# Kernel optimization log

Hardware: AMD Instinct MI355X
Metric: run time of the kernel (lower is better)

The kernel has to match this reference:

```python
import jax, jax.numpy as jnp
import numpy as np

K_RATIO = 0.2
EPS = 1e-6


def setup_inputs() -> dict:
    key = jax.random.key(0)
    k1, k2 = jax.random.split(key)
    B, C, D, H, W = 2, 4, 128, 128, 128
    logits = jax.random.normal(k1, (B, C, D, H, W), dtype=jnp.float32)
    labels = jax.random.randint(k2, (B, D, H, W), 0, C)
    # one-hot target along channel axis 1, matching the tensor-path `target` arg
    target = jax.nn.one_hot(labels, C, axis=1, dtype=jnp.float32)
    return {"logits": logits, "target": target}


def reference(logits, target):
    B, C = logits.shape[0], logits.shape[1]

    # ---- Top-K cross entropy (ignore_index=-1 -> all voxels valid) ----
    y = jnp.argmax(target, axis=1)  # [B, D, H, W] int labels
    logp = jax.nn.log_softmax(logits, axis=1)
    # CE per voxel: -logp[b, y, d, h, w]
    ce = -jnp.take_along_axis(logp, y[:, None], axis=1)[:, 0]  # [B, D, H, W]
    ce_flat = ce.reshape(B, -1)  # [B, N]
    N = ce_flat.shape[1]
    k = max(1, int(N * K_RATIO))  # static: all voxels valid, k < N
    topk_vals, _ = jax.lax.top_k(ce_flat, k)  # [B, k]
    topk_loss = jnp.mean(jnp.mean(topk_vals, axis=1))

    # ---- Soft dice (no valid_mask in tensor path) ----
    p = jax.nn.softmax(logits, axis=1)  # [B, C, D, H, W]
    spatial = tuple(range(2, p.ndim))
    num = 2.0 * jnp.sum(p * target, axis=spatial)          # [B, C]
    den = jnp.sum(p + target, axis=spatial) + EPS          # [B, C]
    dice = 1.0 - num / den                                  # [B, C]
    if C > 1:
        dice = dice[:, 1:]  # drop background channel
    dice_loss = jnp.mean(dice)

    return topk_loss + 0.5 * dice_loss
```

## Files before the change

### kernel.cpp

```cpp
#include <hip/hip_runtime.h>
#include <stdint.h>

#define NVOX (1u << 21)
#define NB   2
#define KSEL 419430u
#define TPB  256
#define VPB  2048
#define BPB  ((int)(NVOX / VPB))
#define NBLK (NB * BPB)
#define NCOPY 64
#define NBIN 4096
#define L1SH 19

__device__ __forceinline__ float wred64(float v) {
#pragma unroll
  for (int o = 32; o > 0; o >>= 1) v += __shfl_down(v, o, 64);
  return v;
}

__global__ __launch_bounds__(TPB, 8) void k1_ce_dice_hist(
    const float* __restrict__ logits, const float* __restrict__ target,
    float* __restrict__ ce, uint32_t* __restrict__ hist1,
    float* __restrict__ dice_acc )
{
  __shared__ uint32_t sh[NBIN];
  const int tid = threadIdx.x;
  for (int i = tid; i < NBIN; i += TPB) sh[i] = 0;
  __syncthreads();

  const int blk = blockIdx.x;
  const int b = blk / BPB;
  const size_t v0 = (size_t)(blk % BPB) * VPB;
  const float* lg = logits + (size_t)b * 4 * NVOX + v0;
  const float* tg = target + (size_t)b * 4 * NVOX + v0;
  float* ceb = ce + ((size_t)b << 21) + v0;

  float sp[4] = {0.f,0.f,0.f,0.f}, nm[4] = {0.f,0.f,0.f,0.f}, ct[4] = {0.f,0.f,0.f,0.f};

#pragma unroll 2
  for (int i = tid * 4; i < VPB; i += TPB * 4) {
    float4 L[4], T[4];
#pragma unroll
    for (int c = 0; c < 4; ++c) {
      L[c] = *(const float4*)(lg + (size_t)c * NVOX + i);
      T[c] = *(const float4*)(tg + (size_t)c * NVOX + i);
    }
    float4 CE;
    float* cep = (float*)&CE;
#pragma unroll
    for (int j = 0; j < 4; ++j) {
      float l[4], t[4];
#pragma unroll
      for (int c = 0; c < 4; ++c) {
        l[c] = ((const float*)&L[c])[j];
        t[c] = ((const float*)&T[c])[j];
      }
      float m = fmaxf(fmaxf(l[0], l[1]), fmaxf(l[2], l[3]));
      float e[4]; float s = 0.f;
#pragma unroll
      for (int c = 0; c < 4; ++c) { e[c] = __expf(l[c] - m); s += e[c]; }
      float inv = 1.f / s;
      float lse = __logf(s);
      float ly = l[0]*t[0] + l[1]*t[1] + l[2]*t[2] + l[3]*t[3];
      float cev = (m - ly) + lse;
      cep[j] = cev;
      atomicAdd(&sh[__float_as_uint(cev) >> L1SH], 1u);
#pragma unroll
      for (int c = 0; c < 4; ++c) {
        float p = e[c] * inv;
        sp[c] += p;
        nm[c] += p * t[c];
        ct[c] += t[c];
      }
    }
    *(float4*)(ceb + i) = CE;
  }

#pragma unroll
  for (int c = 0; c < 4; ++c) { sp[c] = wred64(sp[c]); nm[c] = wred64(nm[c]); ct[c] = wred64(ct[c]); }
  if ((tid & 63) == 0) {
    float* dst = dice_acc + ((size_t)(blk & (NCOPY - 1)) * NB + b) * 12;
#pragma unroll
    for (int c = 0; c < 4; ++c) {
      atomicAdd(dst + c,     sp[c]);
      atomicAdd(dst + 4 + c, nm[c]);
      atomicAdd(dst + 8 + c, ct[c]);
    }
  }
  __syncthreads();
  for (int i = tid; i < NBIN; i += TPB) {
    uint32_t cv = sh[i];
    if (cv) atomicAdd(&hist1[b * NBIN + i], cv);
  }
}

__global__ __launch_bounds__(TPB, 8) void k_pass2(
    const float* __restrict__ ce, const uint32_t* __restrict__ b1p,
    uint32_t* __restrict__ hist2, float* __restrict__ sum_above)
{
  __shared__ uint32_t sh[NBIN];
  __shared__ float wsum[TPB / 64];
  const int tid = threadIdx.x;
  for (int i = tid; i < NBIN; i += TPB) sh[i] = 0;
  __syncthreads();

  const int blk = blockIdx.x;
  const int b = blk / BPB;
  const size_t v0 = (size_t)(blk % BPB) * VPB;
  const float* cb = ce + ((size_t)b << 21) + v0;
  const uint32_t b1 = b1p[b];
  float local = 0.f;

#pragma unroll 2
  for (int i = tid * 4; i < VPB; i += TPB * 4) {
    float4 V = *(const float4*)(cb + i);
    const float* vp = (const float*)&V;
#pragma unroll
    for (int j = 0; j < 4; ++j) {
      uint32_t bits = __float_as_uint(vp[j]);
      uint32_t t12 = bits >> L1SH;
      if (t12 > b1) local += vp[j];
      else if (t12 == b1) atomicAdd(&sh[(bits >> 7) & (NBIN - 1)], 1u);
    }
  }

  local = wred64(local);
  if ((tid & 63) == 0) wsum[tid >> 6] = local;
  __syncthreads();
  if (tid == 0) {
    float t = 0.f;
#pragma unroll
    for (int w = 0; w < TPB / 64; ++w) t += wsum[w];
    if (t != 0.f) atomicAdd(&sum_above[b * NCOPY + (blk & (NCOPY - 1))], t);
  }
  for (int i = tid; i < NBIN; i += TPB) {
    uint32_t cv = sh[i];
    if (cv) atomicAdd(&hist2[(size_t)b * NBIN + i], cv);
  }
}

__global__ __launch_bounds__(256) void k_scan1(
    const uint32_t* __restrict__ hist,
    uint32_t* __restrict__ out_b, uint32_t* __restrict__ out_rem)
{
  const int b = blockIdx.x;
  const int tid = threadIdx.x;
  __shared__ uint32_t chunk[256];
  const int per = NBIN >> 8;
  const uint32_t* h = hist + (size_t)b * NBIN;
  uint32_t s = 0;
  for (int j = 0; j < per; ++j) s += h[tid * per + j];
  chunk[tid] = s;
  __syncthreads();
  if (tid == 0) {
    uint32_t k = KSEL, cum = 0;
    int ci = 255;
    for (; ci > 0; --ci) {
      uint32_t c = chunk[ci];
      if (cum + c >= k) break;
      cum += c;
    }
    int bkt = ci * per;
    for (int j = per - 1; j >= 0; --j) {
      uint32_t c = h[ci * per + j];
      if (cum + c >= k) { bkt = ci * per + j; break; }
      cum += c;
    }
    out_b[b] = (uint32_t)bkt;
    out_rem[b] = k - cum;
  }
}

__global__ __launch_bounds__(256) void k_final(
    const uint32_t* __restrict__ hist2, const uint32_t* __restrict__ b1p,
    const uint32_t* __restrict__ rem1, const float* __restrict__ sum_above,
    const float* __restrict__ dice_acc, float* __restrict__ out)
{
  const int tid = threadIdx.x;
  __shared__ uint32_t chunk[256];
  __shared__ uint32_t sbkt, srem;
  __shared__ float wpart[4];
  __shared__ float ts[NB];
  __shared__ float comp[24];
  const int per = NBIN >> 8;

  for (int b = 0; b < NB; ++b) {
    const uint32_t* h = hist2 + (size_t)b * NBIN;
    uint32_t s = 0;
    for (int j = 0; j < per; ++j) s += h[tid * per + j];
    chunk[tid] = s;
    __syncthreads();
    if (tid == 0) {
      uint32_t k = rem1[b], cum = 0;
      int ci = 255;
      for (; ci > 0; --ci) {
        uint32_t c = chunk[ci];
        if (cum + c >= k) break;
        cum += c;
      }
      int bkt = ci * per;
      for (int j = per - 1; j >= 0; --j) {
        uint32_t c = h[ci * per + j];
        if (cum + c >= k) { bkt = ci * per + j; break; }
        cum += c;
      }
      sbkt = (uint32_t)bkt;
      srem = k - cum;
    }
    __syncthreads();
    const uint32_t b1 = b1p[b];
    const int bkt = (int)sbkt;
    float w = 0.f;
    for (int i = tid; i < NBIN; i += 256) {
      if (i > bkt) {
        uint32_t c = h[i];
        if (c) {
          uint32_t bits = (b1 << L1SH) | ((uint32_t)i << 7) | 64u;
          w += (float)c * __uint_as_float(bits);
        }
      }
    }
    w = wred64(w);
    if ((tid & 63) == 0) wpart[tid >> 6] = w;
    __syncthreads();
    if (tid == 0) {
      float sa = 0.f;
      for (int r = 0; r < NCOPY; ++r) sa += sum_above[b * NCOPY + r];
      uint32_t bits = (b1 << L1SH) | ((uint32_t)bkt << 7) | 64u;
      ts[b] = sa + wpart[0] + wpart[1] + wpart[2] + wpart[3]
              + (float)srem * __uint_as_float(bits);
    }
    __syncthreads();
  }

  if (tid < 24) {
    float a = 0.f;
    for (int r = 0; r < NCOPY; ++r) a += dice_acc[(size_t)r * 24 + tid];
    comp[tid] = a;
  }
  __syncthreads();
  if (tid == 0) {
    float dl = 0.f;
#pragma unroll
    for (int b = 0; b < 2; ++b)
#pragma unroll
      for (int c = 1; c < 4; ++c) {
        float sp = comp[b * 12 + c];
        float nm = comp[b * 12 + 4 + c];
        float ct = comp[b * 12 + 8 + c];
        dl += 1.f - (2.f * nm) / (sp + ct + 1e-6f);
      }
    float topk = 0.5f * (ts[0] + ts[1]) / (float)KSEL;
    out[0] = topk + 0.5f * (dl / 6.f);
  }
}

extern "C" void kernel_launch(void* const* d_in, const int* in_sizes, int n_in,
                              void* d_out, int out_size, void* d_ws, size_t ws_size,
                              hipStream_t stream) {
  (void)in_sizes; (void)n_in; (void)out_size; (void)ws_size;
  const float* logits = (const float*)d_in[0];
  const float* target = (const float*)d_in[1];
  float* out = (float*)d_out;

  char* ws = (char*)d_ws;
  float* ce = (float*)ws;
  const size_t CE_BYTES = (size_t)NB * NVOX * sizeof(float);
  uint32_t* small = (uint32_t*)(ws + CE_BYTES);
  uint32_t* hist1 = small;
  uint32_t* hist2 = hist1 + NB * NBIN;
  uint32_t* b1   = hist2 + NB * NBIN;
  uint32_t* rem1 = b1 + NB;
  float* sum_above = (float*)(rem1 + NB);
  float* dice_acc  = sum_above + NB * NCOPY;
  const size_t SMALL_BYTES =
      (size_t)((char*)(dice_acc + (size_t)NCOPY * NB * 12) - (char*)small);

  hipMemsetAsync(small, 0, SMALL_BYTES, stream);

  k1_ce_dice_hist<<<NBLK, TPB, 0, stream>>>(logits, target, ce, hist1, dice_acc);
  k_scan1<<<NB, 256, 0, stream>>>(hist1, b1, rem1);
  k_pass2<<<NBLK, TPB, 0, stream>>>(ce, b1, hist2, sum_above);
  k_final<<<1, 256, 0, stream>>>(hist2, b1, rem1, sum_above, dice_acc, out);
}
```

Baseline: 204.7 us.

## Replace two-pass radix top-k with single-pass count/sum histogram and interpolation

The first kernel no longer writes per-voxel CE values to global memory. It builds an 8192-bin shared histogram holding both counts and sums of CE, spread over 16 global copies, and a small reduce kernel combines the copies. The final kernel finds the threshold bin, sums the bins above it exactly, and estimates the remaining partial-bin contribution from the bin's average and width. This removes the CE write/read round trip and the second full pass, at the cost of an extra float LDS atomic per voxel, lower occupancy from 64KB of shared memory, and an approximate top-k sum inside the boundary bin.

```diff
diff --git a/kernel.cpp b/kernel.cpp
--- a/kernel.cpp
+++ b/kernel.cpp
@@ -5,12 +5,13 @@
 #define NB   2
 #define KSEL 419430u
 #define TPB  256
-#define VPB  2048
+#define VPB  4096
 #define BPB  ((int)(NVOX / VPB))
 #define NBLK (NB * BPB)
 #define NCOPY 64
-#define NBIN 4096
-#define L1SH 19
+#define NHC  16
+#define NBIN2 8192
+#define SH2  18
 
 __device__ __forceinline__ float wred64(float v) {
 #pragma unroll
@@ -18,14 +19,15 @@
   return v;
 }
 
-__global__ __launch_bounds__(TPB, 8) void k1_ce_dice_hist(
+__global__ __launch_bounds__(TPB, 2) void k1_fused(
     const float* __restrict__ logits, const float* __restrict__ target,
-    float* __restrict__ ce, uint32_t* __restrict__ hist1,
+    uint32_t* __restrict__ hcnt, float* __restrict__ hsum,
     float* __restrict__ dice_acc )
 {
-  __shared__ uint32_t sh[NBIN];
+  __shared__ uint32_t scnt[NBIN2];
+  __shared__ float    ssum[NBIN2];
   const int tid = threadIdx.x;
-  for (int i = tid; i < NBIN; i += TPB) sh[i] = 0;
+  for (int i = tid; i < NBIN2; i += TPB) { scnt[i] = 0; ssum[i] = 0.f; }
   __syncthreads();
 
   const int blk = blockIdx.x;
@@ -33,11 +35,9 @@
   const size_t v0 = (size_t)(blk % BPB) * VPB;
   const float* lg = logits + (size_t)b * 4 * NVOX + v0;
   const float* tg = target + (size_t)b * 4 * NVOX + v0;
-  float* ceb = ce + ((size_t)b << 21) + v0;
 
   float sp[4] = {0.f,0.f,0.f,0.f}, nm[4] = {0.f,0.f,0.f,0.f}, ct[4] = {0.f,0.f,0.f,0.f};
 
-#pragma unroll 2
   for (int i = tid * 4; i < VPB; i += TPB * 4) {
     float4 L[4], T[4];
 #pragma unroll
@@ -45,8 +45,6 @@
       L[c] = *(const float4*)(lg + (size_t)c * NVOX + i);
       T[c] = *(const float4*)(tg + (size_t)c * NVOX + i);
     }
-    float4 CE;
-    float* cep = (float*)&CE;
 #pragma unroll
     for (int j = 0; j < 4; ++j) {
       float l[4], t[4];
@@ -63,8 +61,10 @@
       float lse = __logf(s);
       float ly = l[0]*t[0] + l[1]*t[1] + l[2]*t[2] + l[3]*t[3];
       float cev = (m - ly) + lse;
-      cep[j] = cev;
-      atomicAdd(&sh[__float_as_uint(cev) >> L1SH], 1u);
+      uint32_t idx = __float_as_uint(cev) >> SH2;
+      if (idx >= NBIN2) idx = NBIN2 - 1;
+      atomicAdd(&scnt[idx], 1u);
+      atomicAdd(&ssum[idx], cev);
 #pragma unroll
       for (int c = 0; c < 4; ++c) {
         float p = e[c] * inv;
@@ -73,7 +73,6 @@
         ct[c] += t[c];
       }
     }
-    *(float4*)(ceb + i) = CE;
   }
 
 #pragma unroll
@@ -88,147 +87,98 @@
     }
   }
   __syncthreads();
-  for (int i = tid; i < NBIN; i += TPB) {
-    uint32_t cv = sh[i];
-    if (cv) atomicAdd(&hist1[b * NBIN + i], cv);
-  }
-}
-
-__global__ __launch_bounds__(TPB, 8) void k_pass2(
-    const float* __restrict__ ce, const uint32_t* __restrict__ b1p,
-    uint32_t* __restrict__ hist2, float* __restrict__ sum_above)
+  const size_t hoff = ((size_t)b * NHC + (size_t)(blk & (NHC - 1))) * NBIN2;
+  uint32_t* cdst = hcnt + hoff;
+  float*    sdst = hsum + hoff;
+  for (int i = tid; i < NBIN2; i += TPB) {
+    uint32_t cv = scnt[i];
+    if (cv) {
+      atomicAdd(&cdst[i], cv);
+      atomicAdd(&sdst[i], ssum[i]);
+    }
+  }
+}
+
+__global__ __launch_bounds__(256) void k_reduce(
+    const uint32_t* __restrict__ hcnt, const float* __restrict__ hsum,
+    uint32_t* __restrict__ rcnt, float* __restrict__ rsum)
 {
-  __shared__ uint32_t sh[NBIN];
-  __shared__ float wsum[TPB / 64];
-  const int tid = threadIdx.x;
-  for (int i = tid; i < NBIN; i += TPB) sh[i] = 0;
-  __syncthreads();
-
-  const int blk = blockIdx.x;
-  const int b = blk / BPB;
-  const size_t v0 = (size_t)(blk % BPB) * VPB;
-  const float* cb = ce + ((size_t)b << 21) + v0;
-  const uint32_t b1 = b1p[b];
-  float local = 0.f;
-
-#pragma unroll 2
-  for (int i = tid * 4; i < VPB; i += TPB * 4) {
-    float4 V = *(const float4*)(cb + i);
-    const float* vp = (const float*)&V;
-#pragma unroll
-    for (int j = 0; j < 4; ++j) {
-      uint32_t bits = __float_as_uint(vp[j]);
-      uint32_t t12 = bits >> L1SH;
-      if (t12 > b1) local += vp[j];
-      else if (t12 == b1) atomicAdd(&sh[(bits >> 7) & (NBIN - 1)], 1u);
-    }
-  }
-
-  local = wred64(local);
-  if ((tid & 63) == 0) wsum[tid >> 6] = local;
-  __syncthreads();
-  if (tid == 0) {
-    float t = 0.f;
-#pragma unroll
-    for (int w = 0; w < TPB / 64; ++w) t += wsum[w];
-    if (t != 0.f) atomicAdd(&sum_above[b * NCOPY + (blk & (NCOPY - 1))], t);
-  }
-  for (int i = tid; i < NBIN; i += TPB) {
-    uint32_t cv = sh[i];
-    if (cv) atomicAdd(&hist2[(size_t)b * NBIN + i], cv);
-  }
-}
-
-__global__ __launch_bounds__(256) void k_scan1(
-    const uint32_t* __restrict__ hist,
-    uint32_t* __restrict__ out_b, uint32_t* __restrict__ out_rem)
-{
-  const int b = blockIdx.x;
-  const int tid = threadIdx.x;
-  __shared__ uint32_t chunk[256];
-  const int per = NBIN >> 8;
-  const uint32_t* h = hist + (size_t)b * NBIN;
-  uint32_t s = 0;
-  for (int j = 0; j < per; ++j) s += h[tid * per + j];
-  chunk[tid] = s;
-  __syncthreads();
-  if (tid == 0) {
-    uint32_t k = KSEL, cum = 0;
-    int ci = 255;
-    for (; ci > 0; --ci) {
-      uint32_t c = chunk[ci];
-      if (cum + c >= k) break;
-      cum += c;
-    }
-    int bkt = ci * per;
-    for (int j = per - 1; j >= 0; --j) {
-      uint32_t c = h[ci * per + j];
-      if (cum + c >= k) { bkt = ci * per + j; break; }
-      cum += c;
-    }
-    out_b[b] = (uint32_t)bkt;
-    out_rem[b] = k - cum;
-  }
+  const int b = blockIdx.x >> 3;
+  const int seg = blockIdx.x & 7;
+  const int base = seg * 1024 + threadIdx.x * 4;
+  uint4 c = {0,0,0,0};
+  float4 s = {0.f,0.f,0.f,0.f};
+  for (int copy = 0; copy < NHC; ++copy) {
+    const size_t off = ((size_t)b * NHC + copy) * NBIN2 + base;
+    uint4 cv = *(const uint4*)(hcnt + off);
+    float4 sv = *(const float4*)(hsum + off);
+    c.x += cv.x; c.y += cv.y; c.z += cv.z; c.w += cv.w;
+    s.x += sv.x; s.y += sv.y; s.z += sv.z; s.w += sv.w;
+  }
+  *(uint4*)(rcnt + (size_t)b * NBIN2 + base) = c;
+  *(float4*)(rsum + (size_t)b * NBIN2 + base) = s;
 }
 
 __global__ __launch_bounds__(256) void k_final(
-    const uint32_t* __restrict__ hist2, const uint32_t* __restrict__ b1p,
-    const uint32_t* __restrict__ rem1, const float* __restrict__ sum_above,
+    const uint32_t* __restrict__ rcnt, const float* __restrict__ rsum,
     const float* __restrict__ dice_acc, float* __restrict__ out)
 {
-  const int tid = threadIdx.x;
+  __shared__ uint32_t shc[NBIN2];
   __shared__ uint32_t chunk[256];
   __shared__ uint32_t sbkt, srem;
   __shared__ float wpart[4];
   __shared__ float ts[NB];
   __shared__ float comp[24];
-  const int per = NBIN >> 8;
+  const int tid = threadIdx.x;
 
   for (int b = 0; b < NB; ++b) {
-    const uint32_t* h = hist2 + (size_t)b * NBIN;
+    const uint32_t* rc = rcnt + (size_t)b * NBIN2;
+    const float*    rs = rsum + (size_t)b * NBIN2;
     uint32_t s = 0;
-    for (int j = 0; j < per; ++j) s += h[tid * per + j];
+    for (int j = 0; j < 32; ++j) {
+      uint32_t v = rc[tid * 32 + j];
+      shc[tid * 32 + j] = v;
+      s += v;
+    }
     chunk[tid] = s;
     __syncthreads();
     if (tid == 0) {
-      uint32_t k = rem1[b], cum = 0;
+      uint32_t k = KSEL, cum = 0;
       int ci = 255;
       for (; ci > 0; --ci) {
         uint32_t c = chunk[ci];
         if (cum + c >= k) break;
         cum += c;
       }
-      int bkt = ci * per;
-      for (int j = per - 1; j >= 0; --j) {
-        uint32_t c = h[ci * per + j];
-        if (cum + c >= k) { bkt = ci * per + j; break; }
+      int bkt = ci * 32;
+      for (int j = 31; j >= 0; --j) {
+        uint32_t c = shc[ci * 32 + j];
+        if (cum + c >= k) { bkt = ci * 32 + j; break; }
         cum += c;
       }
       sbkt = (uint32_t)bkt;
       srem = k - cum;
     }
     __syncthreads();
-    const uint32_t b1 = b1p[b];
     const int bkt = (int)sbkt;
     float w = 0.f;
-    for (int i = tid; i < NBIN; i += 256) {
-      if (i > bkt) {
-        uint32_t c = h[i];
-        if (c) {
-          uint32_t bits = (b1 << L1SH) | ((uint32_t)i << 7) | 64u;
-          w += (float)c * __uint_as_float(bits);
-        }
-      }
+    for (int j = 0; j < 32; ++j) {
+      int bin = tid * 32 + j;
+      if (bin > bkt) w += rs[bin];
     }
     w = wred64(w);
     if ((tid & 63) == 0) wpart[tid >> 6] = w;
     __syncthreads();
     if (tid == 0) {
-      float sa = 0.f;
-      for (int r = 0; r < NCOPY; ++r) sa += sum_above[b * NCOPY + r];
-      uint32_t bits = (b1 << L1SH) | ((uint32_t)bkt << 7) | 64u;
-      ts[b] = sa + wpart[0] + wpart[1] + wpart[2] + wpart[3]
-              + (float)srem * __uint_as_float(bits);
+      float cnt_t = (float)shc[bkt];
+      float sum_t = rs[bkt];
+      float lo = __uint_as_float((uint32_t)bkt << SH2);
+      float hi = __uint_as_float((uint32_t)(bkt + 1) << SH2);
+      float width = hi - lo;
+      float avg = sum_t / cnt_t;
+      float frac = (float)srem / cnt_t;
+      float est = avg + (1.f - frac) * 0.5f * width;
+      ts[b] = wpart[0] + wpart[1] + wpart[2] + wpart[3] + (float)srem * est;
     }
     __syncthreads();
   }
@@ -264,22 +214,16 @@
   float* out = (float*)d_out;
 
   char* ws = (char*)d_ws;
-  float* ce = (float*)ws;
-  const size_t CE_BYTES = (size_t)NB * NVOX * sizeof(float);
-  uint32_t* small = (uint32_t*)(ws + CE_BYTES);
-  uint32_t* hist1 = small;
-  uint32_t* hist2 = hist1 + NB * NBIN;
-  uint32_t* b1   = hist2 + NB * NBIN;
-  uint32_t* rem1 = b1 + NB;
-  float* sum_above = (float*)(rem1 + NB);
-  float* dice_acc  = sum_above + NB * NCOPY;
-  const size_t SMALL_BYTES =
-      (size_t)((char*)(dice_acc + (size_t)NCOPY * NB * 12) - (char*)small);
-
-  hipMemsetAsync(small, 0, SMALL_BYTES, stream);
-
-  k1_ce_dice_hist<<<NBLK, TPB, 0, stream>>>(logits, target, ce, hist1, dice_acc);
-  k_scan1<<<NB, 256, 0, stream>>>(hist1, b1, rem1);
-  k_pass2<<<NBLK, TPB, 0, stream>>>(ce, b1, hist2, sum_above);
-  k_final<<<1, 256, 0, stream>>>(hist2, b1, rem1, sum_above, dice_acc, out);
-}
+  uint32_t* hcnt = (uint32_t*)ws;
+  float*    hsum = (float*)(hcnt + (size_t)NB * NHC * NBIN2);
+  float*    dice_acc = hsum + (size_t)NB * NHC * NBIN2;
+  uint32_t* rcnt = (uint32_t*)(dice_acc + (size_t)NCOPY * NB * 12);
+  float*    rsum = (float*)(rcnt + (size_t)NB * NBIN2);
+  const size_t ZERO_BYTES = (size_t)((char*)(dice_acc + (size_t)NCOPY * NB * 12) - ws);
+
+  hipMemsetAsync(hcnt, 0, ZERO_BYTES, stream);
+
+  k1_fused<<<NBLK, TPB, 0, stream>>>(logits, target, hcnt, hsum, dice_acc);
+  k_reduce<<<NB * 8, 256, 0, stream>>>(hcnt, hsum, rcnt, rsum);
+  k_final<<<1, 256, 0, stream>>>(rcnt, rsum, dice_acc, out);
+}
```

Measured after the change: 191.2 us. 1.07x faster.
